# Kernel tuning notes

Hardware: AMD Instinct MI355X
Metric: run time of the kernel (lower is better)

The kernel has to match this reference:

```python
import jax, jax.numpy as jnp
import numpy as np

BLOCK = 128          # block_size in the source
FP8_MAX = 448.0      # max representable magnitude of float8_e4m3fn


def _quant_weight(w):
    """Pre-quantize a [N, K] float weight into fp8 values + per 128x128 block scales."""
    N, K = w.shape
    wb = w.reshape(N // BLOCK, BLOCK, K // BLOCK, BLOCK)
    w_scale = jnp.max(jnp.abs(wb), axis=(1, 3)) / FP8_MAX           # [Nb, Kb]
    s = jnp.where(w_scale == 0, 1.0, w_scale)
    wq = (wb / s[:, None, :, None]).astype(jnp.float8_e4m3fn).astype(jnp.float32)
    return wq.reshape(N, K), w_scale


def setup_inputs() -> dict:
    key = jax.random.key(0)
    kx, kw = jax.random.split(key)
    M, K, N = 16384, 2048, 2048
    x = jax.random.normal(kx, (M, K), dtype=jnp.float32)
    w = jax.random.normal(kw, (N, K), dtype=jnp.float32) * 0.02
    w_fp8, w_scale = _quant_weight(w)
    return {"x": x, "w_fp8": w_fp8, "w_scale": w_scale}


def reference(x, w_fp8, w_scale):
    """fp8 block-quantized linear: act_quant(x) then dequantized GEMM.

    x:       [M, K] float32 activations
    w_fp8:   [N, K] fp8-valued weight (stored as float32, exactly e4m3 representable)
    w_scale: [N/128, K/128] per-block weight scales
    """
    M, K = x.shape
    N = w_fp8.shape[0]
    # --- act_quant: per 128-element block along K, scale = amax / 448 ---
    xb = x.reshape(M, K // BLOCK, BLOCK)
    x_scale = jnp.max(jnp.abs(xb), axis=-1) / FP8_MAX               # [M, Kb]
    sx = jnp.where(x_scale == 0, 1.0, x_scale)
    xq = (xb / sx[..., None]).astype(jnp.float8_e4m3fn).astype(jnp.float32)
    # --- fp8_gemm with inline dequant: scales factor out per (m-block, n-block, k-block)
    # sum_kb sx[m,kb]*sw[nb,kb]*(xq . wq) == (xq*sx) @ (wq*sw)^T exactly ---
    x_deq = (xq * sx[..., None]).reshape(M, K)
    w_deq = (w_fp8.reshape(N // BLOCK, BLOCK, K // BLOCK, BLOCK)
             * w_scale[:, None, :, None]).reshape(N, K)
    return x_deq @ w_deq.T                                          # [M, N]
```

## Files before the change

kernel.cpp:

```cpp
#include <hip/hip_runtime.h>

#define M_DIM 16384
#define N_DIM 2048
#define K_DIM 2048
#define KB    (K_DIM / 128)
#define BM 128
#define BN 128
#define BK 64

typedef __bf16 bf16x8 __attribute__((ext_vector_type(8)));
typedef float  f32x4  __attribute__((ext_vector_type(4)));

__device__ __forceinline__ unsigned short f32_to_bf16_rne(float f) {
    unsigned int u = __float_as_uint(f);
    u += 0x7FFFu + ((u >> 16) & 1u);
    return (unsigned short)(u >> 16);
}

__global__ __launch_bounds__(256) void quant_x_kernel(const float* __restrict__ x,
                                                      unsigned short* __restrict__ xdq) {
    const int gw   = blockIdx.x * 4 + (threadIdx.x >> 6);
    const int lane = threadIdx.x & 63;
    const size_t base = (size_t)gw * 128;
    const float2 v = *(const float2*)(x + base + lane * 2);
    float amax = fmaxf(fabsf(v.x), fabsf(v.y));
#pragma unroll
    for (int m = 32; m >= 1; m >>= 1)
        amax = fmaxf(amax, __shfl_xor(amax, m, 64));
    float s = amax / 448.0f;
    if (s == 0.0f) s = 1.0f;
    const float q0 = v.x / s;
    const float q1 = v.y / s;
    const int p = __builtin_amdgcn_cvt_pk_fp8_f32(q0, q1, 0, false);
    const float d0 = __builtin_amdgcn_cvt_f32_fp8(p, 0) * s;
    const float d1 = __builtin_amdgcn_cvt_f32_fp8(p, 1) * s;
    const unsigned int out = (unsigned int)f32_to_bf16_rne(d0) |
                             ((unsigned int)f32_to_bf16_rne(d1) << 16);
    ((unsigned int*)xdq)[base / 2 + lane] = out;
}

__global__ __launch_bounds__(256) void dequant_w_kernel(const float* __restrict__ w,
                                                        const float* __restrict__ wscale,
                                                        unsigned short* __restrict__ wdq) {
    const size_t e = ((size_t)blockIdx.x * 256 + threadIdx.x) * 2;
    const float2 v = *(const float2*)(w + e);
    const int n = (int)(e >> 11);
    const int k = (int)(e & 2047);
    const float s = wscale[(n >> 7) * KB + (k >> 7)];
    const unsigned int out = (unsigned int)f32_to_bf16_rne(v.x * s) |
                             ((unsigned int)f32_to_bf16_rne(v.y * s) << 16);
    ((unsigned int*)wdq)[e / 2] = out;
}

__global__ __launch_bounds__(256) void gemm_bt_kernel(const unsigned short* __restrict__ A,
                                                      const unsigned short* __restrict__ B,
                                                      float* __restrict__ C) {
    __shared__ __align__(16) unsigned short As[BM * BK];
    __shared__ __align__(16) unsigned short Bs[BN * BK];

    const int tid  = threadIdx.x;
    const int lane = tid & 63;
    const int wave = tid >> 6;
    const int wm   = (wave >> 1) * 64;
    const int wn   = (wave & 1) * 64;
    const int quad = lane >> 4;
    const int l16  = lane & 15;

    const int m0 = blockIdx.y * BM;
    const int n0 = blockIdx.x * BN;

    f32x4 acc[4][4] = {};

    const int srow = tid >> 3;
    const int skc  = tid & 7;
    const unsigned short* gA = A + (size_t)(m0 + srow) * K_DIM + skc * 8;
    const unsigned short* gB = B + (size_t)(n0 + srow) * K_DIM + skc * 8;

    for (int kt = 0; kt < K_DIM / BK; ++kt) {
        const int k0 = kt * BK;
#pragma unroll
        for (int i = 0; i < 4; ++i) {
            __builtin_amdgcn_global_load_lds(
                (__attribute__((address_space(1))) void*)(gA + (size_t)(i * 32) * K_DIM + k0),
                (__attribute__((address_space(3))) void*)(As + (i * 256 + wave * 64) * 8),
                16, 0, 0);
        }
#pragma unroll
        for (int i = 0; i < 4; ++i) {
            __builtin_amdgcn_global_load_lds(
                (__attribute__((address_space(1))) void*)(gB + (size_t)(i * 32) * K_DIM + k0),
                (__attribute__((address_space(3))) void*)(Bs + (i * 256 + wave * 64) * 8),
                16, 0, 0);
        }
        __syncthreads();
#pragma unroll
        for (int ks = 0; ks < BK; ks += 32) {
            bf16x8 af[4], bfr[4];
#pragma unroll
            for (int i = 0; i < 4; ++i)
                af[i] = *(const bf16x8*)(As + (wm + i * 16 + l16) * BK + ks + quad * 8);
#pragma unroll
            for (int j = 0; j < 4; ++j)
                bfr[j] = *(const bf16x8*)(Bs + (wn + j * 16 + l16) * BK + ks + quad * 8);
#pragma unroll
            for (int i = 0; i < 4; ++i)
#pragma unroll
                for (int j = 0; j < 4; ++j)
                    acc[i][j] = __builtin_amdgcn_mfma_f32_16x16x32_bf16(af[i], bfr[j], acc[i][j], 0, 0, 0);
        }
        __syncthreads();
    }

#pragma unroll
    for (int i = 0; i < 4; ++i) {
        const int row = m0 + wm + i * 16 + quad * 4;
#pragma unroll
        for (int j = 0; j < 4; ++j) {
            const int col = n0 + wn + j * 16 + l16;
            float* cp = C + (size_t)row * N_DIM + col;
#pragma unroll
            for (int r = 0; r < 4; ++r)
                cp[(size_t)r * N_DIM] = acc[i][j][r];
        }
    }
}

extern "C" void kernel_launch(void* const* d_in, const int* in_sizes, int n_in,
                              void* d_out, int out_size, void* d_ws, size_t ws_size,
                              hipStream_t stream) {
    const float* x      = (const float*)d_in[0];
    const float* wfp8   = (const float*)d_in[1];
    const float* wscale = (const float*)d_in[2];
    float* out = (float*)d_out;

    unsigned short* xdq = (unsigned short*)d_ws;
    unsigned short* wdq = xdq + (size_t)M_DIM * K_DIM;

    quant_x_kernel<<<(M_DIM * KB) / 4, 256, 0, stream>>>(x, xdq);
    dequant_w_kernel<<<(N_DIM * K_DIM / 2) / 256, 256, 0, stream>>>(wfp8, wscale, wdq);
    gemm_bt_kernel<<<dim3(N_DIM / BN, M_DIM / BM), 256, 0, stream>>>(xdq, wdq, out);
}
```

Baseline: 423.0 us.

## Fuse quant kernels, vectorize to float4, swizzle LDS, swap GEMM grid order

Merges the activation-quant and weight-dequant kernels into one launch, and each thread now handles four elements through float4 loads with a 32-lane amax reduction. The GEMM applies an XOR swizzle to the LDS column chunk, on both the global_load_lds destinations and the fragment reads, to avoid bank conflicts. It also swaps grid x/y so consecutive blocks walk M and share the same B tile. This cuts launch overhead, the LDS conflicts on 128-byte row strides, and the cache locality of the operand tiles, at the cost of more index arithmetic and changed L2 reuse patterns.

```diff
diff --git a/kernel.cpp b/kernel.cpp
--- a/kernel.cpp
+++ b/kernel.cpp
@@ -8,6 +8,9 @@
 #define BN 128
 #define BK 64
 
+#define XGRID (M_DIM * K_DIM / 1024)
+#define WGRID (N_DIM * K_DIM / 1024)
+
 typedef __bf16 bf16x8 __attribute__((ext_vector_type(8)));
 typedef float  f32x4  __attribute__((ext_vector_type(4)));
 
@@ -17,39 +20,42 @@
     return (unsigned short)(u >> 16);
 }
 
-__global__ __launch_bounds__(256) void quant_x_kernel(const float* __restrict__ x,
-                                                      unsigned short* __restrict__ xdq) {
-    const int gw   = blockIdx.x * 4 + (threadIdx.x >> 6);
-    const int lane = threadIdx.x & 63;
-    const size_t base = (size_t)gw * 128;
-    const float2 v = *(const float2*)(x + base + lane * 2);
-    float amax = fmaxf(fabsf(v.x), fabsf(v.y));
-#pragma unroll
-    for (int m = 32; m >= 1; m >>= 1)
-        amax = fmaxf(amax, __shfl_xor(amax, m, 64));
-    float s = amax / 448.0f;
-    if (s == 0.0f) s = 1.0f;
-    const float q0 = v.x / s;
-    const float q1 = v.y / s;
-    const int p = __builtin_amdgcn_cvt_pk_fp8_f32(q0, q1, 0, false);
-    const float d0 = __builtin_amdgcn_cvt_f32_fp8(p, 0) * s;
-    const float d1 = __builtin_amdgcn_cvt_f32_fp8(p, 1) * s;
-    const unsigned int out = (unsigned int)f32_to_bf16_rne(d0) |
-                             ((unsigned int)f32_to_bf16_rne(d1) << 16);
-    ((unsigned int*)xdq)[base / 2 + lane] = out;
-}
-
-__global__ __launch_bounds__(256) void dequant_w_kernel(const float* __restrict__ w,
+__global__ __launch_bounds__(256) void quant_all_kernel(const float* __restrict__ x,
+                                                        unsigned short* __restrict__ xdq,
+                                                        const float* __restrict__ w,
                                                         const float* __restrict__ wscale,
                                                         unsigned short* __restrict__ wdq) {
-    const size_t e = ((size_t)blockIdx.x * 256 + threadIdx.x) * 2;
-    const float2 v = *(const float2*)(w + e);
-    const int n = (int)(e >> 11);
-    const int k = (int)(e & 2047);
-    const float s = wscale[(n >> 7) * KB + (k >> 7)];
-    const unsigned int out = (unsigned int)f32_to_bf16_rne(v.x * s) |
-                             ((unsigned int)f32_to_bf16_rne(v.y * s) << 16);
-    ((unsigned int*)wdq)[e / 2] = out;
+    const int tid = threadIdx.x;
+    if (blockIdx.x < XGRID) {
+        const size_t base = ((size_t)blockIdx.x * 256 + tid) * 4;
+        const float4 v = *(const float4*)(x + base);
+        float amax = fmaxf(fmaxf(fabsf(v.x), fabsf(v.y)), fmaxf(fabsf(v.z), fabsf(v.w)));
+#pragma unroll
+        for (int m = 16; m >= 1; m >>= 1)
+            amax = fmaxf(amax, __shfl_xor(amax, m, 64));
+        float s = amax / 448.0f;
+        if (s == 0.0f) s = 1.0f;
+        const int p01 = __builtin_amdgcn_cvt_pk_fp8_f32(v.x / s, v.y / s, 0, false);
+        const int p23 = __builtin_amdgcn_cvt_pk_fp8_f32(v.z / s, v.w / s, 0, false);
+        const float d0 = __builtin_amdgcn_cvt_f32_fp8(p01, 0) * s;
+        const float d1 = __builtin_amdgcn_cvt_f32_fp8(p01, 1) * s;
+        const float d2 = __builtin_amdgcn_cvt_f32_fp8(p23, 0) * s;
+        const float d3 = __builtin_amdgcn_cvt_f32_fp8(p23, 1) * s;
+        uint2 out;
+        out.x = (unsigned int)f32_to_bf16_rne(d0) | ((unsigned int)f32_to_bf16_rne(d1) << 16);
+        out.y = (unsigned int)f32_to_bf16_rne(d2) | ((unsigned int)f32_to_bf16_rne(d3) << 16);
+        *(uint2*)(xdq + base) = out;
+    } else {
+        const size_t e = ((size_t)(blockIdx.x - XGRID) * 256 + tid) * 4;
+        const float4 v = *(const float4*)(w + e);
+        const int n = (int)(e >> 11);
+        const int k = (int)(e & 2047);
+        const float s = wscale[(n >> 7) * KB + (k >> 7)];
+        uint2 out;
+        out.x = (unsigned int)f32_to_bf16_rne(v.x * s) | ((unsigned int)f32_to_bf16_rne(v.y * s) << 16);
+        out.y = (unsigned int)f32_to_bf16_rne(v.z * s) | ((unsigned int)f32_to_bf16_rne(v.w * s) << 16);
+        *(uint2*)(wdq + e) = out;
+    }
 }
 
 __global__ __launch_bounds__(256) void gemm_bt_kernel(const unsigned short* __restrict__ A,
@@ -66,15 +72,15 @@
     const int quad = lane >> 4;
     const int l16  = lane & 15;
 
-    const int m0 = blockIdx.y * BM;
-    const int n0 = blockIdx.x * BN;
+    const int m0 = blockIdx.x * BM;
+    const int n0 = blockIdx.y * BN;
 
     f32x4 acc[4][4] = {};
 
     const int srow = tid >> 3;
-    const int skc  = tid & 7;
-    const unsigned short* gA = A + (size_t)(m0 + srow) * K_DIM + skc * 8;
-    const unsigned short* gB = B + (size_t)(n0 + srow) * K_DIM + skc * 8;
+    const int scol = (tid & 7) ^ (srow & 7);
+    const unsigned short* gA = A + (size_t)(m0 + srow) * K_DIM + scol * 8;
+    const unsigned short* gB = B + (size_t)(n0 + srow) * K_DIM + scol * 8;
 
     for (int kt = 0; kt < K_DIM / BK; ++kt) {
         const int k0 = kt * BK;
@@ -95,13 +101,15 @@
         __syncthreads();
 #pragma unroll
         for (int ks = 0; ks < BK; ks += 32) {
+            const int c = (ks >> 3) + quad;
+            const int swz = (c ^ (l16 & 7)) * 8;
             bf16x8 af[4], bfr[4];
 #pragma unroll
             for (int i = 0; i < 4; ++i)
-                af[i] = *(const bf16x8*)(As + (wm + i * 16 + l16) * BK + ks + quad * 8);
+                af[i] = *(const bf16x8*)(As + (wm + i * 16 + l16) * BK + swz);
 #pragma unroll
             for (int j = 0; j < 4; ++j)
-                bfr[j] = *(const bf16x8*)(Bs + (wn + j * 16 + l16) * BK + ks + quad * 8);
+                bfr[j] = *(const bf16x8*)(Bs + (wn + j * 16 + l16) * BK + swz);
 #pragma unroll
             for (int i = 0; i < 4; ++i)
 #pragma unroll
@@ -136,7 +144,6 @@
     unsigned short* xdq = (unsigned short*)d_ws;
     unsigned short* wdq = xdq + (size_t)M_DIM * K_DIM;
 
-    quant_x_kernel<<<(M_DIM * KB) / 4, 256, 0, stream>>>(x, xdq);
-    dequant_w_kernel<<<(N_DIM * K_DIM / 2) / 256, 256, 0, stream>>>(wfp8, wscale, wdq);
-    gemm_bt_kernel<<<dim3(N_DIM / BN, M_DIM / BM), 256, 0, stream>>>(xdq, wdq, out);
+    quant_all_kernel<<<XGRID + WGRID, 256, 0, stream>>>(x, xdq, wfp8, wscale, wdq);
+    gemm_bt_kernel<<<dim3(M_DIM / BM, N_DIM / BN), 256, 0, stream>>>(xdq, wdq, out);
 }
```

Measured after the change: 373.0 us. -11.8%, faster.
